# Performance work log

Hardware: AMD Instinct MI355X
Metric: run time of the kernel (lower is better)

## Reference

```python
import jax, jax.numpy as jnp
import numpy as np

CH = 256   # backbone feature channels
HID = 10   # ConvLSTM hidden dim
B, H, W = 8, 128, 128


def _leaf_gates(cc):
    # cc: [..., 3*HID, H, W] -> (h, c) each [..., HID, H, W]
    i, o, g = jnp.split(cc, 3, axis=-3)
    c = jax.nn.sigmoid(i) * jnp.tanh(g)
    h = jax.nn.sigmoid(o) * jnp.tanh(c)
    return h, c


def _tree_cell(x, h_ch, c_ch, Wg, Wf):
    # x: [B, CH+1, H, W]; h_ch, c_ch: [K, B, HID, H, W]
    # child-sum Tree-ConvLSTM with 1x1 convs (bias=False)
    h_sum = h_ch.sum(0)
    cc = (jnp.einsum('oc,bchw->bohw', Wg[:, :CH + 1], x)
          + jnp.einsum('oc,bchw->bohw', Wg[:, CH + 1:], h_sum))  # [B,3*HID,H,W]
    i, o, g = jnp.split(cc, 3, axis=1)
    # per-child forget gates
    fx = jnp.einsum('oc,bchw->bohw', Wf[:, :CH + 1], x)          # [B,HID,H,W]
    fh = jnp.einsum('oc,kbchw->kbohw', Wf[:, CH + 1:], h_ch)     # [K,B,HID,H,W]
    f = jax.nn.sigmoid(fx[None] + fh)
    c = jax.nn.sigmoid(i) * jnp.tanh(g) + (f * c_ch).sum(0)
    h = jax.nn.sigmoid(o) * jnp.tanh(c)
    return h, c


def setup_inputs() -> dict:
    key = jax.random.key(0)
    ks = jax.random.split(key, 13)
    s = 0.05  # keep gate pre-activations in a sane range
    return {
        'seg_p': jax.random.uniform(ks[0], (B, 7, H, W), jnp.float32),
        'seg_h': jax.random.uniform(ks[1], (B, 3, H, W), jnp.float32),
        'seg_f': jax.random.uniform(ks[2], (B, 2, H, W), jnp.float32),
        'p_fea': jax.random.normal(ks[3], (B, CH, H, W), jnp.float32),
        'h_fea': jax.random.normal(ks[4], (B, CH, H, W), jnp.float32),
        'f_fea': jax.random.normal(ks[5], (B, CH, H, W), jnp.float32),
        'W_leaf': jax.random.normal(ks[6], (6, 3 * HID, CH + 1), jnp.float32) * s,
        'W_up': jax.random.normal(ks[7], (3 * HID, CH + 1 + HID), jnp.float32) * s,
        'Wf_up': jax.random.normal(ks[8], (HID, CH + 1 + HID), jnp.float32) * s,
        'W_low': jax.random.normal(ks[9], (3 * HID, CH + 1 + HID), jnp.float32) * s,
        'Wf_low': jax.random.normal(ks[10], (HID, CH + 1 + HID), jnp.float32) * s,
        'W_full': jax.random.normal(ks[11], (3 * HID, CH + 1 + HID), jnp.float32) * s,
        'Wf_full': jax.random.normal(ks[12], (HID, CH + 1 + HID), jnp.float32) * s,
    }


def reference(seg_p, seg_h, seg_f, p_fea, h_fea, f_fea,
              W_leaf, W_up, Wf_up, W_low, Wf_low, W_full, Wf_full):
    # --- 6 leaf ConvLSTM cells (cls_p-1), input = cat([p_fea, seg_p[:, i+1]]) ---
    # Split the 1x1 conv into the shared 256-ch part and the per-cell seg channel.
    cc = (jnp.einsum('noc,bchw->nbohw', W_leaf[:, :, :CH], p_fea)
          + jnp.einsum('no,bnhw->nbohw', W_leaf[:, :, CH], seg_p[:, 1:7]))  # [6,B,30,H,W]
    half_h, half_c = _leaf_gates(cc)  # each [6,B,HID,H,W]

    # --- half upper (children 1..4) and lower (children 5..6) tree cells ---
    x_up = jnp.concatenate([h_fea, seg_h[:, 1:2]], axis=1)
    x_low = jnp.concatenate([h_fea, seg_h[:, 2:3]], axis=1)
    up_h, up_c = _tree_cell(x_up, half_h[:4], half_c[:4], W_up, Wf_up)
    low_h, low_c = _tree_cell(x_low, half_h[4:], half_c[4:], W_low, Wf_low)

    # --- full body tree cell (note: original passes lower h twice) ---
    x_full = jnp.concatenate([f_fea, seg_f[:, 1:2]], axis=1)
    full_h, full_c = _tree_cell(x_full,
                                jnp.stack([low_h, low_h]),
                                jnp.stack([up_c, low_c]),
                                W_full, Wf_full)

    # Flatten the original output structure (6 h + 2 half h + full h + 6 c + 2 half c + full c)
    out = jnp.concatenate([
        half_h, low_h[None], low_h[None], full_h[None],
        half_c, up_c[None], low_c[None], full_c[None],
    ], axis=0)  # [18, B, HID, H, W]
    return out
```

## Files before the change

### kernel.cpp

```cpp
#include <hip/hip_runtime.h>

namespace {

constexpr int kHW  = 128 * 128;
constexpr int kCH  = 256;
constexpr int kHID = 10;
constexpr int kB   = 8;

typedef __attribute__((ext_vector_type(8))) short bf16x8;
typedef __attribute__((ext_vector_type(4))) float f32x4;

constexpr int kSegOffL   = 80 * 512;
constexpr int kLdsBytesL = kSegOffL + 20 * 4 * 4;

constexpr int kSideOffU2 = 128 * 512;
constexpr int kSideOffF2 = kSideOffU2 + 80 * 11 * 4;
constexpr int kXchOff    = kSideOffF2 + 48 * 11 * 4;
constexpr int kLdsBytesUF = kXchOff + 8 * 16 * 20 * 4;

__device__ __forceinline__ float sigm(float x) {
    return __builtin_amdgcn_rcpf(1.0f + __expf(-x));
}
__device__ __forceinline__ float tanh_(float x) {
    return 1.0f - 2.0f * __builtin_amdgcn_rcpf(__expf(2.0f * x) + 1.0f);
}
__device__ __forceinline__ unsigned short bf16b(float f) {
    unsigned u = __float_as_uint(f);
    return (unsigned short)((u + 0x7FFFu + ((u >> 16) & 1u)) >> 16);
}
__device__ __forceinline__ bf16x8 cvt8(const float* v) {
    union { unsigned u[4]; bf16x8 h; } r;
    #pragma unroll
    for (int i = 0; i < 4; ++i)
        asm("v_cvt_pk_bf16_f32 %0, %1, %2"
            : "=v"(r.u[i]) : "v"(v[2 * i]), "v"(v[2 * i + 1]));
    return r.h;
}

#define LOADF(base, step)                                                  \
    { const float* p_ = (base) + (step) * 32 * kHW;                        \
      _Pragma("unroll") for (int c_ = 0; c_ < 4; ++c_)                     \
      _Pragma("unroll") for (int j_ = 0; j_ < 8; ++j_)                     \
          nf[c_][j_] = p_[c_ * 16 + j_ * kHW]; }

#define CVT4()                                                             \
    { _Pragma("unroll") for (int c_ = 0; c_ < 4; ++c_) bc[c_] = cvt8(nf[c_]); }

__global__ __launch_bounds__(256, 3) void k_leaf_mfma(
    const float* __restrict__ p_fea,
    const float* __restrict__ seg_p,
    const float* __restrict__ W_leaf,
    float* __restrict__ out)
{
    extern __shared__ char smem[];
    const int tid   = threadIdx.x;
    const int bid   = blockIdx.x;
    const int group = bid / 24;
    const int rem   = bid - group * 24;
    const int cls   = rem >> 3;
    const int tile  = group * 8 + (rem & 7);

    for (int idx = tid; idx < 2 * 30 * 257; idx += 256) {
        const int np   = idx / 7710;
        const int rrem = idx - np * 7710;
        const int orow = rrem / 257;
        const int c    = rrem - orow * 257;
        const int g    = orow / 10;
        const int q    = orow - g * 10;
        const int slot = (g == 0) ? 0 : (g == 1 ? 2 : 1);
        const int t    = np * 10 + q;
        const float v  = W_leaf[(cls * 2 + np) * 7710 + rrem];
        if (c == 256) {
            ((float*)(smem + kSegOffL))[t * 4 + slot] = v;
        } else {
            const int row  = t * 4 + slot;
            const int byte = row * 512 + ((2 * c) ^ ((row & 7) << 4));
            *(unsigned short*)(smem + byte) = bf16b(v);
        }
    }
    for (int i = tid; i < 20 * 128; i += 256) {
        const int t = i >> 7, d = i & 127;
        *(unsigned*)(smem + (t * 4 + 3) * 512 + d * 4) = 0u;
    }
    if (tid < 20) ((float*)(smem + kSegOffL))[tid * 4 + 3] = 0.f;
    __syncthreads();

    const int w  = tid >> 6;
    const int ln = tid & 63;
    const int lr = ln & 15;
    const int lg = ln >> 4;

    const int b    = tile >> 6;
    const int hw0  = (tile & 63) * 256;
    const int col0 = hw0 + w * 64 + lr;
    const float* bbase = p_fea + b * kCH * kHW + lg * 8 * kHW + col0;

    f32x4 acc[5][4];
    #pragma unroll
    for (int m = 0; m < 5; ++m)
        #pragma unroll
        for (int c = 0; c < 4; ++c) {
            acc[m][c][0] = 0.f; acc[m][c][1] = 0.f;
            acc[m][c][2] = 0.f; acc[m][c][3] = 0.f;
        }

    float nf[4][8];
    bf16x8 bc[4];
    LOADF(bbase, 0)
    CVT4()
    LOADF(bbase, 1)

    #pragma unroll
    for (int ks = 0; ks < 8; ++ks) {
        const int kb = (ks * 32 + lg * 8) * 2;
        #pragma unroll
        for (int m = 0; m < 5; ++m) {
            const int row = m * 16 + lr;
            const bf16x8 a = *(const bf16x8*)(
                smem + row * 512 + (kb ^ ((row & 7) << 4)));
            #pragma unroll
            for (int c = 0; c < 4; ++c)
                acc[m][c] = __builtin_amdgcn_mfma_f32_16x16x32_bf16(a, bc[c], acc[m][c], 0, 0, 0);
        }
        if (ks < 7) {
            CVT4()
            if (ks < 6) LOADF(bbase, ks + 2)
        }
    }

    #pragma unroll
    for (int m = 0; m < 5; ++m) {
        const int t = m * 4 + lg;
        const int n = cls * 2 + t / 10;
        const int q = t % 10;
        const float4 sw = *(const float4*)(smem + kSegOffL + t * 16);
        const float* sp = seg_p + (b * 7 + n + 1) * kHW;
        float* oh = out + ((n * kB + b) * kHID + q) * kHW;
        float* oc = out + (((9 + n) * kB + b) * kHID + q) * kHW;
        #pragma unroll
        for (int ct = 0; ct < 4; ++ct) {
            const int px = col0 + ct * 16;
            const float sg = sp[px];
            const float ci = acc[m][ct][0] + sw.x * sg;
            const float cg = acc[m][ct][1] + sw.y * sg;
            const float co = acc[m][ct][2] + sw.z * sg;
            const float c  = sigm(ci) * tanh_(cg);
            const float h  = sigm(co) * tanh_(c);
            oh[px] = h;
            oc[px] = c;
        }
    }
}

__global__ __launch_bounds__(256, 2) void k_uplow_full_mfma(
    const float* __restrict__ h_fea,
    const float* __restrict__ f_fea,
    const float* __restrict__ seg_h,
    const float* __restrict__ seg_f,
    const float* __restrict__ W_up,    const float* __restrict__ Wf_up,
    const float* __restrict__ W_low,   const float* __restrict__ Wf_low,
    const float* __restrict__ W_full,  const float* __restrict__ Wf_full,
    float* __restrict__ out)
{
    extern __shared__ char smem[];
    const int tid = threadIdx.x;

    for (int idx = tid; idx < 128 * 267; idx += 256) {
        const int row = idx / 267;
        const int c   = idx - row * 267;
        float v = 0.f;
        if (row < 80) {
            const int t = row >> 2, slot = row & 3;
            if (t < 10) {
                if      (slot == 0) v = W_up[t * 267 + c];
                else if (slot == 1) v = W_up[(20 + t) * 267 + c];
                else if (slot == 2) v = Wf_up[t * 267 + c];
            } else {
                const int q = t - 10;
                if      (slot == 0) v = W_low[q * 267 + c];
                else if (slot == 1) v = W_low[(20 + q) * 267 + c];
                else if (slot == 2) v = W_low[(10 + q) * 267 + c];
                else                v = Wf_low[q * 267 + c];
            }
        } else {
            const int r2 = row - 80;
            const int t = r2 >> 2, slot = r2 & 3;
            if (t < 10) {
                if      (slot == 0) v = W_full[t * 267 + c];
                else if (slot == 1) v = W_full[(20 + t) * 267 + c];
                else if (slot == 2) v = W_full[(10 + t) * 267 + c];
                else                v = Wf_full[t * 267 + c];
                if (c >= 257 && slot < 3) v *= 2.0f;
            }
        }
        if (c < 256) {
            const int byte = row * 512 + ((2 * c) ^ ((row & 7) << 4));
            *(unsigned short*)(smem + byte) = bf16b(v);
        } else if (row < 80) {
            ((float*)(smem + kSideOffU2))[row * 11 + (c - 256)] = v;
        } else {
            ((float*)(smem + kSideOffF2))[(row - 80) * 11 + (c - 256)] = v;
        }
    }
    __syncthreads();

    const int w  = tid >> 6;
    const int ln = tid & 63;
    const int lr = ln & 15;
    const int lg = ln >> 4;
    const float* sideU = (const float*)(smem + kSideOffU2);
    const float* sideF = (const float*)(smem + kSideOffF2);
    float* xch = (float*)(smem + kXchOff) + w * 320 + lr * 20;

    const int tix  = blockIdx.x;
    const int b    = tix >> 6;
    const int hw0  = (tix & 63) * 256;
    const int col0 = hw0 + w * 64 + lr;
    const float* bbaseH = h_fea + b * kCH * kHW + lg * 8 * kHW + col0;
    const float* bbaseF = f_fea + b * kCH * kHW + lg * 8 * kHW + col0;

    f32x4 acc[5][4];
    #pragma unroll
    for (int m = 0; m < 5; ++m)
        #pragma unroll
        for (int c = 0; c < 4; ++c) {
            acc[m][c][0] = 0.f; acc[m][c][1] = 0.f;
            acc[m][c][2] = 0.f; acc[m][c][3] = 0.f;
        }
    f32x4 accF[3][4];
    #pragma unroll
    for (int m = 0; m < 3; ++m)
        #pragma unroll
        for (int c = 0; c < 4; ++c) {
            accF[m][c][0] = 0.f; accF[m][c][1] = 0.f;
            accF[m][c][2] = 0.f; accF[m][c][3] = 0.f;
        }

    float nf[4][8];
    bf16x8 bc[4];

    LOADF(bbaseH, 0)
    CVT4()
    LOADF(bbaseH, 1)
    #pragma unroll
    for (int ks = 0; ks < 8; ++ks) {
        const int kb = (ks * 32 + lg * 8) * 2;
        #pragma unroll
        for (int m = 0; m < 5; ++m) {
            const int row = m * 16 + lr;
            const bf16x8 a = *(const bf16x8*)(
                smem + row * 512 + (kb ^ ((row & 7) << 4)));
            #pragma unroll
            for (int c = 0; c < 4; ++c)
                acc[m][c] = __builtin_amdgcn_mfma_f32_16x16x32_bf16(a, bc[c], acc[m][c], 0, 0, 0);
        }
        if (ks < 7) {
            CVT4()
            if (ks < 6) LOADF(bbaseH, ks + 2)
        }
    }

    LOADF(bbaseF, 0)
    CVT4()
    LOADF(bbaseF, 1)
    #pragma unroll
    for (int ks = 0; ks < 8; ++ks) {
        const int kb = (ks * 32 + lg * 8) * 2;
        #pragma unroll
        for (int m = 0; m < 3; ++m) {
            const int row = 80 + m * 16 + lr;
            const bf16x8 a = *(const bf16x8*)(
                smem + row * 512 + (kb ^ ((row & 7) << 4)));
            #pragma unroll
            for (int c = 0; c < 4; ++c)
                accF[m][c] = __builtin_amdgcn_mfma_f32_16x16x32_bf16(a, bc[c], accF[m][c], 0, 0, 0);
        }
        if (ks < 7) {
            CVT4()
            if (ks < 6) LOADF(bbaseF, ks + 2)
        }
    }

    __syncthreads();
    {
        char* stBase = smem + w * 15360;
        #pragma unroll
        for (int n = 0; n < 6; ++n) {
            #pragma unroll
            for (int j = 0; j < 10; ++j) {
                const float* g = out + ((n * kB + b) * kHID + j) * kHW + hw0 + w * 64 + ln;
                __builtin_amdgcn_global_load_lds(
                    (const __attribute__((address_space(1))) unsigned*)g,
                    (__attribute__((address_space(3))) unsigned*)(stBase + (n * 10 + j) * 256),
                    4, 0, 0);
            }
        }
        asm volatile("s_waitcnt vmcnt(0)" ::: "memory");
        __builtin_amdgcn_sched_barrier(0);
    }
    const float* stW = (const float*)(smem + w * 15360);

    #pragma unroll
    for (int ct = 0; ct < 4; ++ct) {
        const int px = col0 + ct * 16;
        const int ix = lr + ct * 16;

        const float sU = seg_h[(b * 3 + 1) * kHW + px];
        const float sL = seg_h[(b * 3 + 2) * kHW + px];
        const float sF = seg_f[(b * 2 + 1) * kHW + px];

        float hsU[10], hsL[10];
        #pragma unroll
        for (int j = 0; j < 10; ++j) {
            hsU[j] = stW[(0 * 10 + j) * 64 + ix] + stW[(1 * 10 + j) * 64 + ix]
                   + stW[(2 * 10 + j) * 64 + ix] + stW[(3 * 10 + j) * 64 + ix];
            hsL[j] = stW[(4 * 10 + j) * 64 + ix] + stW[(5 * 10 + j) * 64 + ix];
        }

        float ucv[3] = {0.f, 0.f, 0.f};

        #pragma unroll
        for (int m = 0; m < 5; ++m) {
            const int t = m * 4 + lg;
            if (t < 10) {
                float ai = acc[m][ct][0] + sideU[(t * 4 + 0) * 11] * sU;
                float ag = acc[m][ct][1] + sideU[(t * 4 + 1) * 11] * sU;
                const float pf = acc[m][ct][2] + sideU[(t * 4 + 2) * 11] * sU;
                float cs = 0.f;
                #pragma unroll
                for (int n = 0; n < 4; ++n) {
                    float fh = pf;
                    #pragma unroll
                    for (int j = 0; j < 10; ++j)
                        fh = fmaf(sideU[(t * 4 + 2) * 11 + 1 + j],
                                  stW[(n * 10 + j) * 64 + ix], fh);
                    const float cv = out[(((9 + n) * kB + b) * kHID + t) * kHW + px];
                    cs = fmaf(sigm(fh), cv, cs);
                }
                #pragma unroll
                for (int j = 0; j < 10; ++j) {
                    ai = fmaf(sideU[(t * 4 + 0) * 11 + 1 + j], hsU[j], ai);
                    ag = fmaf(sideU[(t * 4 + 1) * 11 + 1 + j], hsU[j], ag);
                }
                const float uc = sigm(ai) * tanh_(ag) + cs;
                out[((15 * kB + b) * kHID + t) * kHW + px] = uc;
                if (m < 3) ucv[m] = uc;
            } else {
                const int q = t - 10;
                float ai = acc[m][ct][0] + sideU[(t * 4 + 0) * 11] * sL;
                float ag = acc[m][ct][1] + sideU[(t * 4 + 1) * 11] * sL;
                float ao = acc[m][ct][2] + sideU[(t * 4 + 2) * 11] * sL;
                const float pf = acc[m][ct][3] + sideU[(t * 4 + 3) * 11] * sL;
                float cs = 0.f;
                #pragma unroll
                for (int n = 4; n < 6; ++n) {
                    float fh = pf;
                    #pragma unroll
                    for (int j = 0; j < 10; ++j)
                        fh = fmaf(sideU[(t * 4 + 3) * 11 + 1 + j],
                                  stW[(n * 10 + j) * 64 + ix], fh);
                    const float cv = out[(((9 + n) * kB + b) * kHID + q) * kHW + px];
                    cs = fmaf(sigm(fh), cv, cs);
                }
                #pragma unroll
                for (int j = 0; j < 10; ++j) {
                    ai = fmaf(sideU[(t * 4 + 0) * 11 + 1 + j], hsL[j], ai);
                    ag = fmaf(sideU[(t * 4 + 1) * 11 + 1 + j], hsL[j], ag);
                    ao = fmaf(sideU[(t * 4 + 2) * 11 + 1 + j], hsL[j], ao);
                }
                const float lcv = sigm(ai) * tanh_(ag) + cs;
                const float lhv = sigm(ao) * tanh_(lcv);
                out[((6 * kB + b) * kHID + q) * kHW + px]  = lhv;
                out[((7 * kB + b) * kHID + q) * kHW + px]  = lhv;
                out[((16 * kB + b) * kHID + q) * kHW + px] = lcv;
                xch[q]      = lhv;
                xch[10 + q] = lcv;
            }
        }

        asm volatile("s_waitcnt lgkmcnt(0)" ::: "memory");
        __builtin_amdgcn_sched_barrier(0);

        float lhx[10];
        #pragma unroll
        for (int j = 0; j < 10; ++j) lhx[j] = xch[j];

        #pragma unroll
        for (int mf = 0; mf < 3; ++mf) {
            const int t = mf * 4 + lg;
            if (t < 10) {
                float ai = accF[mf][ct][0] + sideF[(t * 4 + 0) * 11] * sF;
                float ag = accF[mf][ct][1] + sideF[(t * 4 + 1) * 11] * sF;
                float ao = accF[mf][ct][2] + sideF[(t * 4 + 2) * 11] * sF;
                float fh = accF[mf][ct][3] + sideF[(t * 4 + 3) * 11] * sF;
                #pragma unroll
                for (int j = 0; j < 10; ++j) {
                    ai = fmaf(sideF[(t * 4 + 0) * 11 + 1 + j], lhx[j], ai);
                    ag = fmaf(sideF[(t * 4 + 1) * 11 + 1 + j], lhx[j], ag);
                    ao = fmaf(sideF[(t * 4 + 2) * 11 + 1 + j], lhx[j], ao);
                    fh = fmaf(sideF[(t * 4 + 3) * 11 + 1 + j], lhx[j], fh);
                }
                const float lcx = xch[10 + t];
                const float cf = sigm(ai) * tanh_(ag) + sigm(fh) * (ucv[mf] + lcx);
                const float hv = sigm(ao) * tanh_(cf);
                out[((8 * kB + b) * kHID + t) * kHW + px]  = hv;
                out[((17 * kB + b) * kHID + t) * kHW + px] = cf;
            }
        }
    }
}

}

extern "C" void kernel_launch(void* const* d_in, const int* in_sizes, int n_in,
                              void* d_out, int out_size, void* d_ws, size_t ws_size,
                              hipStream_t stream) {
    const float* seg_p   = (const float*)d_in[0];
    const float* seg_h   = (const float*)d_in[1];
    const float* seg_f   = (const float*)d_in[2];
    const float* p_fea   = (const float*)d_in[3];
    const float* h_fea   = (const float*)d_in[4];
    const float* f_fea   = (const float*)d_in[5];
    const float* W_leaf  = (const float*)d_in[6];
    const float* W_up    = (const float*)d_in[7];
    const float* Wf_up   = (const float*)d_in[8];
    const float* W_low   = (const float*)d_in[9];
    const float* Wf_low  = (const float*)d_in[10];
    const float* W_full  = (const float*)d_in[11];
    const float* Wf_full = (const float*)d_in[12];
    float* out = (float*)d_out;

    (void)hipFuncSetAttribute(reinterpret_cast<const void*>(k_uplow_full_mfma),
                              hipFuncAttributeMaxDynamicSharedMemorySize, kLdsBytesUF);

    hipLaunchKernelGGL(k_leaf_mfma, dim3(3 * 512), dim3(256), kLdsBytesL, stream,
                       p_fea, seg_p, W_leaf, out);
    hipLaunchKernelGGL(k_uplow_full_mfma, dim3(512), dim3(256), kLdsBytesUF, stream,
                       h_fea, f_fea, seg_h, seg_f,
                       W_up, Wf_up, W_low, Wf_low, W_full, Wf_full, out);
}
```

Measured before the change: 256.5 us.

## Stage leaf c states in LDS too and split epilogue staging into two phases

The epilogue used to stage only the six leaf h planes into LDS and read the leaf c values for the forget-gate sum directly from global memory, one scattered load per term. It now stages both h and c (120 rows) via global_load_lds in two 32-column phases, so each phase fits the existing per-wave LDS region. The seg values are now loaded before the wait. This targets the scattered global c loads and latency stalls in the epilogue, at the cost of an extra LDS wait and more load instructions per phase.

```diff
diff --git a/kernel.cpp b/kernel.cpp
--- a/kernel.cpp
+++ b/kernel.cpp
@@ -282,129 +282,149 @@
     }
 
     __syncthreads();
-    {
-        char* stBase = smem + w * 15360;
-        #pragma unroll
-        for (int n = 0; n < 6; ++n) {
-            #pragma unroll
-            for (int j = 0; j < 10; ++j) {
-                const float* g = out + ((n * kB + b) * kHID + j) * kHW + hw0 + w * 64 + ln;
-                __builtin_amdgcn_global_load_lds(
-                    (const __attribute__((address_space(1))) unsigned*)g,
-                    (__attribute__((address_space(3))) unsigned*)(stBase + (n * 10 + j) * 256),
-                    4, 0, 0);
-            }
+    char* stBase = smem + w * 15360;
+    const float* stR = (const float*)stBase;
+    const int rowHalf = ln >> 5;
+    const int colL    = ln & 31;
+
+    #pragma unroll
+    for (int phase = 0; phase < 2; ++phase) {
+        if (phase == 1) {
+            asm volatile("s_waitcnt lgkmcnt(0)" ::: "memory");
+            __builtin_amdgcn_sched_barrier(0);
+        }
+        const int ctBase = phase * 32;
+        #pragma unroll
+        for (int k = 0; k < 60; ++k) {
+            const int row = 2 * k + rowHalf;
+            int gi;
+            if (row < 60) {
+                gi = ((row / 10) * kB + b) * kHID + (row % 10);
+            } else {
+                const int r2 = row - 60;
+                gi = (((r2 / 10) + 9) * kB + b) * kHID + (r2 % 10);
+            }
+            const float* g = out + (size_t)gi * kHW + hw0 + w * 64 + ctBase + colL;
+            __builtin_amdgcn_global_load_lds(
+                (const __attribute__((address_space(1))) unsigned*)g,
+                (__attribute__((address_space(3))) unsigned*)(stBase + k * 256),
+                4, 0, 0);
+        }
+        float sUv[2], sLv[2], sFv[2];
+        #pragma unroll
+        for (int cti = 0; cti < 2; ++cti) {
+            const int px = col0 + (phase * 2 + cti) * 16;
+            sUv[cti] = seg_h[(b * 3 + 1) * kHW + px];
+            sLv[cti] = seg_h[(b * 3 + 2) * kHW + px];
+            sFv[cti] = seg_f[(b * 2 + 1) * kHW + px];
         }
         asm volatile("s_waitcnt vmcnt(0)" ::: "memory");
         __builtin_amdgcn_sched_barrier(0);
-    }
-    const float* stW = (const float*)(smem + w * 15360);
-
-    #pragma unroll
-    for (int ct = 0; ct < 4; ++ct) {
-        const int px = col0 + ct * 16;
-        const int ix = lr + ct * 16;
-
-        const float sU = seg_h[(b * 3 + 1) * kHW + px];
-        const float sL = seg_h[(b * 3 + 2) * kHW + px];
-        const float sF = seg_f[(b * 2 + 1) * kHW + px];
-
-        float hsU[10], hsL[10];
-        #pragma unroll
-        for (int j = 0; j < 10; ++j) {
-            hsU[j] = stW[(0 * 10 + j) * 64 + ix] + stW[(1 * 10 + j) * 64 + ix]
-                   + stW[(2 * 10 + j) * 64 + ix] + stW[(3 * 10 + j) * 64 + ix];
-            hsL[j] = stW[(4 * 10 + j) * 64 + ix] + stW[(5 * 10 + j) * 64 + ix];
-        }
-
-        float ucv[3] = {0.f, 0.f, 0.f};
-
-        #pragma unroll
-        for (int m = 0; m < 5; ++m) {
-            const int t = m * 4 + lg;
-            if (t < 10) {
-                float ai = acc[m][ct][0] + sideU[(t * 4 + 0) * 11] * sU;
-                float ag = acc[m][ct][1] + sideU[(t * 4 + 1) * 11] * sU;
-                const float pf = acc[m][ct][2] + sideU[(t * 4 + 2) * 11] * sU;
-                float cs = 0.f;
-                #pragma unroll
-                for (int n = 0; n < 4; ++n) {
-                    float fh = pf;
+
+        #pragma unroll
+        for (int cti = 0; cti < 2; ++cti) {
+            const int ct  = phase * 2 + cti;
+            const int px  = col0 + ct * 16;
+            const int ixl = lr + cti * 16;
+            const float sU = sUv[cti], sL = sLv[cti], sF = sFv[cti];
+
+            float hsU[10], hsL[10];
+            #pragma unroll
+            for (int j = 0; j < 10; ++j) {
+                hsU[j] = stR[(0 * 10 + j) * 32 + ixl] + stR[(1 * 10 + j) * 32 + ixl]
+                       + stR[(2 * 10 + j) * 32 + ixl] + stR[(3 * 10 + j) * 32 + ixl];
+                hsL[j] = stR[(4 * 10 + j) * 32 + ixl] + stR[(5 * 10 + j) * 32 + ixl];
+            }
+
+            float ucv[3] = {0.f, 0.f, 0.f};
+
+            #pragma unroll
+            for (int m = 0; m < 5; ++m) {
+                const int t = m * 4 + lg;
+                if (t < 10) {
+                    float ai = acc[m][ct][0] + sideU[(t * 4 + 0) * 11] * sU;
+                    float ag = acc[m][ct][1] + sideU[(t * 4 + 1) * 11] * sU;
+                    const float pf = acc[m][ct][2] + sideU[(t * 4 + 2) * 11] * sU;
+                    float cs = 0.f;
                     #pragma unroll
-                    for (int j = 0; j < 10; ++j)
-                        fh = fmaf(sideU[(t * 4 + 2) * 11 + 1 + j],
-                                  stW[(n * 10 + j) * 64 + ix], fh);
-                    const float cv = out[(((9 + n) * kB + b) * kHID + t) * kHW + px];
-                    cs = fmaf(sigm(fh), cv, cs);
+                    for (int n = 0; n < 4; ++n) {
+                        float fh = pf;
+                        #pragma unroll
+                        for (int j = 0; j < 10; ++j)
+                            fh = fmaf(sideU[(t * 4 + 2) * 11 + 1 + j],
+                                      stR[(n * 10 + j) * 32 + ixl], fh);
+                        const float cv = stR[(60 + n * 10 + t) * 32 + ixl];
+                        cs = fmaf(sigm(fh), cv, cs);
+                    }
+                    #pragma unroll
+                    for (int j = 0; j < 10; ++j) {
+                        ai = fmaf(sideU[(t * 4 + 0) * 11 + 1 + j], hsU[j], ai);
+                        ag = fmaf(sideU[(t * 4 + 1) * 11 + 1 + j], hsU[j], ag);
+                    }
+                    const float uc = sigm(ai) * tanh_(ag) + cs;
+                    out[((15 * kB + b) * kHID + t) * kHW + px] = uc;
+                    if (m < 3) ucv[m] = uc;
+                } else {
+                    const int q = t - 10;
+                    float ai = acc[m][ct][0] + sideU[(t * 4 + 0) * 11] * sL;
+                    float ag = acc[m][ct][1] + sideU[(t * 4 + 1) * 11] * sL;
+                    float ao = acc[m][ct][2] + sideU[(t * 4 + 2) * 11] * sL;
+                    const float pf = acc[m][ct][3] + sideU[(t * 4 + 3) * 11] * sL;
+                    float cs = 0.f;
+                    #pragma unroll
+                    for (int n = 4; n < 6; ++n) {
+                        float fh = pf;
+                        #pragma unroll
+                        for (int j = 0; j < 10; ++j)
+                            fh = fmaf(sideU[(t * 4 + 3) * 11 + 1 + j],
+                                      stR[(n * 10 + j) * 32 + ixl], fh);
+                        const float cv = stR[(60 + n * 10 + q) * 32 + ixl];
+                        cs = fmaf(sigm(fh), cv, cs);
+                    }
+                    #pragma unroll
+                    for (int j = 0; j < 10; ++j) {
+                        ai = fmaf(sideU[(t * 4 + 0) * 11 + 1 + j], hsL[j], ai);
+                        ag = fmaf(sideU[(t * 4 + 1) * 11 + 1 + j], hsL[j], ag);
+                        ao = fmaf(sideU[(t * 4 + 2) * 11 + 1 + j], hsL[j], ao);
+                    }
+                    const float lcv = sigm(ai) * tanh_(ag) + cs;
+                    const float lhv = sigm(ao) * tanh_(lcv);
+                    out[((6 * kB + b) * kHID + q) * kHW + px]  = lhv;
+                    out[((7 * kB + b) * kHID + q) * kHW + px]  = lhv;
+                    out[((16 * kB + b) * kHID + q) * kHW + px] = lcv;
+                    xch[q]      = lhv;
+                    xch[10 + q] = lcv;
                 }
-                #pragma unroll
-                for (int j = 0; j < 10; ++j) {
-                    ai = fmaf(sideU[(t * 4 + 0) * 11 + 1 + j], hsU[j], ai);
-                    ag = fmaf(sideU[(t * 4 + 1) * 11 + 1 + j], hsU[j], ag);
+            }
+
+            asm volatile("s_waitcnt lgkmcnt(0)" ::: "memory");
+            __builtin_amdgcn_sched_barrier(0);
+
+            float lhx[10];
+            #pragma unroll
+            for (int j = 0; j < 10; ++j) lhx[j] = xch[j];
+
+            #pragma unroll
+            for (int mf = 0; mf < 3; ++mf) {
+                const int t = mf * 4 + lg;
+                if (t < 10) {
+                    float ai = accF[mf][ct][0] + sideF[(t * 4 + 0) * 11] * sF;
+                    float ag = accF[mf][ct][1] + sideF[(t * 4 + 1) * 11] * sF;
+                    float ao = accF[mf][ct][2] + sideF[(t * 4 + 2) * 11] * sF;
+                    float fh = accF[mf][ct][3] + sideF[(t * 4 + 3) * 11] * sF;
+                    #pragma unroll
+                    for (int j = 0; j < 10; ++j) {
+                        ai = fmaf(sideF[(t * 4 + 0) * 11 + 1 + j], lhx[j], ai);
+                        ag = fmaf(sideF[(t * 4 + 1) * 11 + 1 + j], lhx[j], ag);
+                        ao = fmaf(sideF[(t * 4 + 2) * 11 + 1 + j], lhx[j], ao);
+                        fh = fmaf(sideF[(t * 4 + 3) * 11 + 1 + j], lhx[j], fh);
+                    }
+                    const float lcx = xch[10 + t];
+                    const float cf = sigm(ai) * tanh_(ag) + sigm(fh) * (ucv[mf] + lcx);
+                    const float hv = sigm(ao) * tanh_(cf);
+                    out[((8 * kB + b) * kHID + t) * kHW + px]  = hv;
+                    out[((17 * kB + b) * kHID + t) * kHW + px] = cf;
                 }
-                const float uc = sigm(ai) * tanh_(ag) + cs;
-                out[((15 * kB + b) * kHID + t) * kHW + px] = uc;
-                if (m < 3) ucv[m] = uc;
-            } else {
-                const int q = t - 10;
-                float ai = acc[m][ct][0] + sideU[(t * 4 + 0) * 11] * sL;
-                float ag = acc[m][ct][1] + sideU[(t * 4 + 1) * 11] * sL;
-                float ao = acc[m][ct][2] + sideU[(t * 4 + 2) * 11] * sL;
-                const float pf = acc[m][ct][3] + sideU[(t * 4 + 3) * 11] * sL;
-                float cs = 0.f;
-                #pragma unroll
-                for (int n = 4; n < 6; ++n) {
-                    float fh = pf;
-                    #pragma unroll
-                    for (int j = 0; j < 10; ++j)
-                        fh = fmaf(sideU[(t * 4 + 3) * 11 + 1 + j],
-                                  stW[(n * 10 + j) * 64 + ix], fh);
-                    const float cv = out[(((9 + n) * kB + b) * kHID + q) * kHW + px];
-                    cs = fmaf(sigm(fh), cv, cs);
-                }
-                #pragma unroll
-                for (int j = 0; j < 10; ++j) {
-                    ai = fmaf(sideU[(t * 4 + 0) * 11 + 1 + j], hsL[j], ai);
-                    ag = fmaf(sideU[(t * 4 + 1) * 11 + 1 + j], hsL[j], ag);
-                    ao = fmaf(sideU[(t * 4 + 2) * 11 + 1 + j], hsL[j], ao);
-                }
-                const float lcv = sigm(ai) * tanh_(ag) + cs;
-                const float lhv = sigm(ao) * tanh_(lcv);
-                out[((6 * kB + b) * kHID + q) * kHW + px]  = lhv;
-                out[((7 * kB + b) * kHID + q) * kHW + px]  = lhv;
-                out[((16 * kB + b) * kHID + q) * kHW + px] = lcv;
-                xch[q]      = lhv;
-                xch[10 + q] = lcv;
-            }
-        }
-
-        asm volatile("s_waitcnt lgkmcnt(0)" ::: "memory");
-        __builtin_amdgcn_sched_barrier(0);
-
-        float lhx[10];
-        #pragma unroll
-        for (int j = 0; j < 10; ++j) lhx[j] = xch[j];
-
-        #pragma unroll
-        for (int mf = 0; mf < 3; ++mf) {
-            const int t = mf * 4 + lg;
-            if (t < 10) {
-                float ai = accF[mf][ct][0] + sideF[(t * 4 + 0) * 11] * sF;
-                float ag = accF[mf][ct][1] + sideF[(t * 4 + 1) * 11] * sF;
-                float ao = accF[mf][ct][2] + sideF[(t * 4 + 2) * 11] * sF;
-                float fh = accF[mf][ct][3] + sideF[(t * 4 + 3) * 11] * sF;
-                #pragma unroll
-                for (int j = 0; j < 10; ++j) {
-                    ai = fmaf(sideF[(t * 4 + 0) * 11 + 1 + j], lhx[j], ai);
-                    ag = fmaf(sideF[(t * 4 + 1) * 11 + 1 + j], lhx[j], ag);
-                    ao = fmaf(sideF[(t * 4 + 2) * 11 + 1 + j], lhx[j], ao);
-                    fh = fmaf(sideF[(t * 4 + 3) * 11 + 1 + j], lhx[j], fh);
-                }
-                const float lcx = xch[10 + t];
-                const float cf = sigm(ai) * tanh_(ag) + sigm(fh) * (ucv[mf] + lcx);
-                const float hv = sigm(ao) * tanh_(cf);
-                out[((8 * kB + b) * kHID + t) * kHW + px]  = hv;
-                out[((17 * kB + b) * kHID + t) * kHW + px] = cf;
             }
         }
     }
```

Result: slower. 298.7 us (+16.4%).
